# Optimization experiments

Measured on AMD Instinct MI355X. Metric: run time of the kernel, lower is better.

## Reference

```python
import jax, jax.numpy as jnp
import numpy as np

H = 1024          # hidden_size
NH = 16           # num_attention_heads
HD = H // NH      # attention_head_size
EPS = 1e-12       # layer_norm_eps
NEG = jnp.finfo(jnp.float32).min


def setup_inputs() -> dict:
    key = jax.random.key(0)
    ks = jax.random.split(key, 12)
    B, S = 4, 2048
    sc = 1.0 / np.sqrt(H)
    return {
        "hidden_states": jax.random.normal(ks[0], (B, S, H), jnp.float32),
        "attention_mask": jnp.ones((B, S), jnp.float32),
        "Wq": jax.random.normal(ks[1], (H, H), jnp.float32) * sc,
        "bq": jnp.zeros((H,), jnp.float32),
        "Wk": jax.random.normal(ks[2], (H, H), jnp.float32) * sc,
        "bk": jnp.zeros((H,), jnp.float32),
        "Wv": jax.random.normal(ks[3], (H, H), jnp.float32) * sc,
        "bv": jnp.zeros((H,), jnp.float32),
        "Wo": jax.random.normal(ks[4], (H, H), jnp.float32) * sc,
        "bo": jnp.zeros((H,), jnp.float32),
        "ln_g": jnp.ones((H,), jnp.float32),
        "ln_b": jnp.zeros((H,), jnp.float32),
    }


def _split_heads(x):
    # (B, S, H) -> (B, NH, S, HD)
    B, S, _ = x.shape
    return x.reshape(B, S, NH, HD).transpose(0, 2, 1, 3)


def reference(hidden_states, attention_mask, Wq, bq, Wk, bk, Wv, bv, Wo, bo, ln_g, ln_b):
    q = _split_heads(hidden_states @ Wq + bq)
    k = _split_heads(hidden_states @ Wk + bk)
    v = _split_heads(hidden_states @ Wv + bv)

    # (B, NH, S, S)
    scores = jnp.einsum('bhqd,bhkd->bhqk', q, k) / jnp.sqrt(jnp.float32(HD))
    mask_add = (1.0 - attention_mask)[:, None, None, :] * NEG
    scores = scores + mask_add
    probs = jax.nn.softmax(scores, axis=-1)  # dropout is identity (eval / p=0)

    ctx = jnp.einsum('bhqk,bhkd->bhqd', probs, v)
    B, _, S, _ = ctx.shape
    ctx = ctx.transpose(0, 2, 1, 3).reshape(B, S, H)

    out = ctx @ Wo + bo
    x = out + hidden_states
    mu = jnp.mean(x, axis=-1, keepdims=True)
    var = jnp.var(x, axis=-1, keepdims=True)
    return (x - mu) * jax.lax.rsqrt(var + EPS) * ln_g + ln_b
```

## Files before the change

kernel.cpp:

```cpp
#include <hip/hip_runtime.h>
#include <stdint.h>

#define H_ 1024
#define NH_ 16
#define HD_ 64
#define B_ 4
#define S_ 2048
#define M_ (B_*S_)

typedef unsigned short u16;
typedef __attribute__((ext_vector_type(4))) unsigned short u16x4;
typedef __attribute__((ext_vector_type(8))) short bf16x8;
typedef __attribute__((ext_vector_type(4))) float f32x4;
typedef __attribute__((ext_vector_type(16))) float f32x16;
typedef __attribute__((ext_vector_type(4))) unsigned int u32x4;
typedef __attribute__((ext_vector_type(4))) int i32x4;

#define AS1 __attribute__((address_space(1)))
#define AS3 __attribute__((address_space(3)))

__device__ __forceinline__ void gload16(const void* g, void* l) {
  __builtin_amdgcn_global_load_lds((const AS1 void*)g, (AS3 void*)l, 16, 0, 0);
}

__device__ __forceinline__ u16 f2bf(float f) {
  union { float f; uint32_t u; } v; v.f = f;
  uint32_t u = v.u + 0x7FFFu + ((v.u >> 16) & 1u);
  return (u16)(u >> 16);
}

static __device__ __forceinline__ f32x4 mfma16(bf16x8 a, bf16x8 b, f32x4 c) {
  return __builtin_amdgcn_mfma_f32_16x16x32_bf16(a, b, c, 0, 0, 0);
}
static __device__ __forceinline__ f32x16 mfma32(bf16x8 a, bf16x8 b, f32x16 c) {
  return __builtin_amdgcn_mfma_f32_32x32x16_bf16(a, b, c, 0, 0, 0);
}

__device__ __forceinline__ int cvtpk(float lo, float hi) {
  int r;
  asm("v_cvt_pk_bf16_f32 %0, %1, %2" : "=v"(r) : "v"(lo), "v"(hi));
  return r;
}
__device__ __forceinline__ void plswap(int& a, int& b) {
  asm volatile("v_permlane32_swap_b32 %0, %1" : "+v"(a), "+v"(b));
}
#if __has_builtin(__builtin_amdgcn_exp2f)
#define EXP2F __builtin_amdgcn_exp2f
#else
#define EXP2F exp2f
#endif

__device__ __forceinline__ int xcd_swz(int bid, int nwg) {
  return (bid & 7) * (nwg >> 3) + (bid >> 3);
}


__global__ __launch_bounds__(256) void prep_kernel(const float* __restrict__ in, u16* __restrict__ out,
                                                   const float* __restrict__ mask, float* __restrict__ madd_g,
                                                   uint32_t* __restrict__ nzbits,
                                                   const float* __restrict__ Wq, const float* __restrict__ Wk,
                                                   const float* __restrict__ Wv, const float* __restrict__ Wo,
                                                   u16* __restrict__ wt) {
  __shared__ float tile[64][65];
  const int bid = blockIdx.x, t = threadIdx.x;
  if (bid < 4096) {
    int i = bid * 256 + t;
    const f32x4* p = (const f32x4*)in;
    f32x4 a = p[2*i], b = p[2*i+1];
    u32x4 o;
    o.x = (uint32_t)f2bf(a.x) | ((uint32_t)f2bf(a.y) << 16);
    o.y = (uint32_t)f2bf(a.z) | ((uint32_t)f2bf(a.w) << 16);
    o.z = (uint32_t)f2bf(b.x) | ((uint32_t)f2bf(b.y) << 16);
    o.w = (uint32_t)f2bf(b.z) | ((uint32_t)f2bf(b.w) << 16);
    ((u32x4*)out)[i] = o;
  } else if (bid < 4100) {
    const int mb = bid - 4096;
    int i = mb * 256 + t;
    f32x4 a = ((const f32x4*)mask)[2*i], b4 = ((const f32x4*)mask)[2*i+1];
    f32x4 ma, mb4;
    ma.x = (1.0f - a.x) * -3.0e38f;  ma.y = (1.0f - a.y) * -3.0e38f;
    ma.z = (1.0f - a.z) * -3.0e38f;  ma.w = (1.0f - a.w) * -3.0e38f;
    mb4.x = (1.0f - b4.x) * -3.0e38f; mb4.y = (1.0f - b4.y) * -3.0e38f;
    mb4.z = (1.0f - b4.z) * -3.0e38f; mb4.w = (1.0f - b4.w) * -3.0e38f;
    ((f32x4*)madd_g)[2*i] = ma;  ((f32x4*)madd_g)[2*i+1] = mb4;
    if (mb == 0) {
      if (t < B_) nzbits[t] = 0u;
      __syncthreads();
      if (t < B_*32) {
        int b = t >> 5, kt = t & 31;
        const float* mrow = mask + (size_t)b * S_ + kt*64;
        uint32_t nz = 0;
        for (int c = 0; c < 64; ++c) nz |= (mrow[c] != 1.0f) ? 1u : 0u;
        if (nz) atomicOr(&nzbits[b], 1u << kt);
      }
    }
  } else {
    const int w = bid - 4100;
    const int p = w >> 8, ti = w & 255, tr = ti >> 4, tc = ti & 15;
    const float* W = (p == 0) ? Wq : (p == 1) ? Wk : (p == 2) ? Wv : Wo;
#pragma unroll
    for (int it = 0; it < 16; ++it) {
      int idx = it * 256 + t, r = idx >> 6, c = idx & 63;
      tile[r][c] = W[(size_t)(tr*64 + r) * H_ + tc*64 + c];
    }
    __syncthreads();
    u16* outp = wt + (size_t)p * H_ * H_;
#pragma unroll
    for (int it = 0; it < 16; ++it) {
      int idx = it * 256 + t, r = idx >> 6, c = idx & 63;
      outp[(size_t)(tc*64 + r) * H_ + tr*64 + c] = f2bf(tile[c][r]);
    }
  }
}


__device__ __forceinline__ void gemm_tile(const u16* __restrict__ A, const u16* __restrict__ Bt,
                                          int m0, int n0, u16* As, u16* Bs, f32x4 acc[4][4]) {
  const int tid = threadIdx.x;
  const int lane = tid & 63, wave = tid >> 6;
  const int wr = wave >> 1, wc = wave & 1;
  const int l15 = lane & 15, l4 = lane >> 4;
  const int rdx = l15 & 7;
#define GSTAGE(bb, k0) do { \
    _Pragma("unroll") \
    for (int i = 0; i < 4; ++i) { \
      int c = i*256 + tid, row = c >> 3, ch = c & 7; \
      int so = (k0) + ((ch ^ (row & 7)) * 8);    \
      gload16(A + (size_t)(m0 + row) * H_ + so, As + (bb)*8192 + (size_t)c * 8); \
      gload16(Bt + (size_t)(n0 + row) * H_ + so, Bs + (bb)*8192 + (size_t)c * 8); \
    } \
  } while (0)
  GSTAGE(0, 0);
  for (int kt = 0; kt < 16; ++kt) {
    const int cur = kt & 1;
    const int nk = ((kt + 1) & 15) * 64;
    GSTAGE(cur ^ 1, nk);
    asm volatile("s_waitcnt vmcnt(8)\n\ts_barrier" ::: "memory");
    const u16* Ab = As + cur*8192;
    const u16* Bb = Bs + cur*8192;
#pragma unroll
    for (int ks = 0; ks < 2; ++ks) {
      bf16x8 afr[4], bfr[4];
#pragma unroll
      for (int m = 0; m < 4; ++m)
        afr[m] = *(const bf16x8*)&Ab[(wr*64 + m*16 + l15)*64 + (((ks*4 + l4) ^ rdx) * 8)];
#pragma unroll
      for (int n = 0; n < 4; ++n)
        bfr[n] = *(const bf16x8*)&Bb[(wc*64 + n*16 + l15)*64 + (((ks*4 + l4) ^ rdx) * 8)];
#pragma unroll
      for (int m = 0; m < 4; ++m)
#pragma unroll
        for (int n = 0; n < 4; ++n)
          acc[m][n] = mfma16(afr[m], bfr[n], acc[m][n]);
    }
    asm volatile("s_barrier" ::: "memory");
  }
  asm volatile("s_waitcnt vmcnt(0)" ::: "memory");
#undef GSTAGE
}

__global__ __launch_bounds__(256) void gemm_qkv_kernel(const u16* __restrict__ hs16, const u16* __restrict__ wt,
                                                       const float* __restrict__ bq, const float* __restrict__ bk,
                                                       const float* __restrict__ bv, u16* __restrict__ qkv16) {
  __shared__ __align__(16) u16 As[2*128*64], Bs[2*128*64];
  f32x4 acc[4][4] = {};
  const int lg = xcd_swz(blockIdx.x, 1536);
  const int m0 = (lg / 24) * 128, n0 = (lg % 24) * 128;
  gemm_tile(hs16, wt, m0, n0, As, Bs, acc);
  const int tid = threadIdx.x, lane = tid & 63, wave = tid >> 6;
  const int wr = wave >> 1, wc = wave & 1, l15 = lane & 15, l4 = lane >> 4;
  const int p = n0 >> 10;
  const float* bias = (p == 0) ? bq : (p == 1) ? bk : bv;
  const float qsc = (p == 0) ? 0.18033688f : 1.0f;
  u16* base = qkv16 + (size_t)p * ((size_t)B_*NH_*S_*HD_);
  if (p == 2) {
    const int b = m0 >> 11;
#pragma unroll
    for (int n = 0; n < 4; ++n) {
      int ncol = (n0 & 1023) + wc*64 + n*16 + l15;
      int h = ncol >> 6, d = ncol & 63;
      float bsv = bias[ncol];
#pragma unroll
      for (int m = 0; m < 4; ++m) {
        int s0 = (m0 & 2047) + wr*64 + m*16 + l4*4;
        u16x4 pk;
#pragma unroll
        for (int r = 0; r < 4; ++r) pk[r] = f2bf(acc[m][n][r] + bsv);
        *(u16x4*)(base + (((size_t)b*NH_ + h)*HD_ + d)*S_ + s0) = pk;
      }
    }
  } else {
#pragma unroll
    for (int n = 0; n < 4; ++n) {
      int ncol = (n0 & 1023) + wc*64 + n*16 + l15;
      int h = ncol >> 6, d = ncol & 63;
      float bsv = bias[ncol];
#pragma unroll
      for (int m = 0; m < 4; ++m) {
#pragma unroll
        for (int r = 0; r < 4; ++r) {
          int row = m0 + wr*64 + m*16 + l4*4 + r;
          int b = row >> 11, s = row & 2047;
          base[(((size_t)b*NH_ + h)*S_ + s)*HD_ + d] = f2bf((acc[m][n][r] + bsv) * qsc);
        }
      }
    }
  }
}

__global__ __launch_bounds__(256) void gemm_out_kernel(const u16* __restrict__ ctx16, const u16* __restrict__ wo,
                                                       const float* __restrict__ bo, const float* __restrict__ hs,
                                                       float* __restrict__ xout) {
  __shared__ __align__(16) u16 As[2*128*64], Bs[2*128*64];
  f32x4 acc[4][4] = {};
  const int lg = xcd_swz(blockIdx.x, 512);
  const int m0 = (lg / 8) * 128, n0 = (lg % 8) * 128;
  gemm_tile(ctx16, wo, m0, n0, As, Bs, acc);
  const int tid = threadIdx.x, lane = tid & 63, wave = tid >> 6;
  const int wr = wave >> 1, wc = wave & 1, l15 = lane & 15, l4 = lane >> 4;
#pragma unroll
  for (int n = 0; n < 4; ++n) {
    int col = n0 + wc*64 + n*16 + l15;
    float bsv = bo[col];
#pragma unroll
    for (int m = 0; m < 4; ++m) {
#pragma unroll
      for (int r = 0; r < 4; ++r) {
        int row = m0 + wr*64 + m*16 + l4*4 + r;
        size_t off = (size_t)row * H_ + col;
        xout[off] = acc[m][n][r] + bsv + hs[off];
      }
    }
  }
}


__global__ __launch_bounds__(256, 2) void attn_kernel(const u16* __restrict__ q_, const u16* __restrict__ k_,
                                                      const u16* __restrict__ vt_, const float* __restrict__ madd_g,
                                                      const uint32_t* __restrict__ nzbits,
                                                      u16* __restrict__ ctx16) {
  __shared__ __align__(16) u16 Ks[2][64*64], Vs[2][64*64];
  __shared__ __align__(16) float Sc[4][64];
  const int lgid = xcd_swz(blockIdx.x, 512);
  const int qb = lgid & 7, bh = lgid >> 3, h = bh & 15, b = bh >> 4;
  const int tid = threadIdx.x, lane = tid & 63, wave = tid >> 6;
  const int l31 = lane & 31, hi = lane >> 5;
  const size_t headoff = ((size_t)b * NH_ + h) * ((size_t)S_ * HD_);
  const u16* Q  = q_ + headoff;
  const u16* K  = k_ + headoff;
  const u16* Vt = vt_ + headoff;
  const uint32_t nzb = nzbits[b];
  const int qbase = qb*256 + wave*64;
  bf16x8 qfA[4], qfB[4];
#pragma unroll
  for (int st = 0; st < 4; ++st) {
    qfA[st] = *(const bf16x8*)(Q + (size_t)(qbase + l31) * HD_ + st*16 + hi*8);
    qfB[st] = *(const bf16x8*)(Q + (size_t)(qbase + 32 + l31) * HD_ + st*16 + hi*8);
  }
  f32x16 O00 = {}, O01 = {}, O10 = {}, O11 = {};
  float lA = 0.f, lB = 0.f;
  const int srow = tid >> 3, sch = tid & 7;
  const int gch = sch ^ (srow & 7);
  const int swzA = l31 & 7;

#define STAGE(bb, kt) do { \
    const u16* Kt_ = K + (size_t)(kt) * 64 * HD_; \
    _Pragma("unroll") \
    for (int c = 0; c < 2; ++c) { \
      int row = c*32 + srow; \
      gload16(Kt_ + (size_t)row * HD_ + gch*8, &Ks[bb][c*2048 + (size_t)tid*8]); \
      gload16(Vt + (size_t)row * S_ + (kt)*64 + gch*8, &Vs[bb][c*2048 + (size_t)tid*8]); \
    } \
  } while (0)

  STAGE(0, 0);
  __syncthreads();

  for (int kt = 0; kt < 32; ++kt) {
    const int cur = kt & 1;
    const int nxt = (kt + 1) & 31;
    STAGE(cur ^ 1, nxt);
    asm volatile("s_waitcnt vmcnt(4)\n\ts_barrier" ::: "memory");
    f32x16 sA0 = {}, sA1 = {}, sB0 = {}, sB1 = {};
    __builtin_amdgcn_s_setprio(1);
#pragma unroll
    for (int st = 0; st < 4; ++st) {
      const int kch = ((2*st + hi) ^ swzA) * 8;
      bf16x8 kf0 = *(const bf16x8*)&Ks[cur][l31*64 + kch];
      bf16x8 kf1 = *(const bf16x8*)&Ks[cur][(32 + l31)*64 + kch];
      sA0 = mfma32(kf0, qfA[st], sA0);
      sA1 = mfma32(kf1, qfA[st], sA1);
      sB0 = mfma32(kf0, qfB[st], sB0);
      sB1 = mfma32(kf1, qfB[st], sB1);
    }
    __builtin_amdgcn_s_setprio(0);
    if ((nzb >> kt) & 1u) {
#pragma unroll
      for (int t = 0; t < 2; ++t) {
        f32x16& sa = t ? sA1 : sA0;
        f32x16& sb2 = t ? sB1 : sB0;
#pragma unroll
        for (int bq = 0; bq < 4; ++bq) {
          f32x4 md = *(const f32x4*)(madd_g + (size_t)b * S_ + kt*64 + t*32 + bq*8 + hi*4);
#pragma unroll
          for (int a = 0; a < 4; ++a) { sa[bq*4 + a] += md[a]; sb2[bq*4 + a] += md[a]; }
        }
      }
    }
#pragma unroll
    for (int r = 0; r < 16; ++r) sA0[r] = EXP2F(sA0[r]);
#pragma unroll
    for (int r = 0; r < 16; ++r) sA1[r] = EXP2F(sA1[r]);
#pragma unroll
    for (int r = 0; r < 16; ++r) sB0[r] = EXP2F(sB0[r]);
#pragma unroll
    for (int r = 0; r < 16; ++r) sB1[r] = EXP2F(sB1[r]);
    {
      float v[16];
#pragma unroll
      for (int r = 0; r < 16; ++r) v[r] = sA0[r] + sA1[r];
#pragma unroll
      for (int r = 0; r < 8; ++r) v[r] += v[r+8];
#pragma unroll
      for (int r = 0; r < 4; ++r) v[r] += v[r+4];
      float rs_ = (v[0] + v[1]) + (v[2] + v[3]);
      int a0 = __float_as_int(rs_), b0 = a0; plswap(a0, b0);
      lA += __int_as_float(a0) + __int_as_float(b0);
#pragma unroll
      for (int r = 0; r < 16; ++r) v[r] = sB0[r] + sB1[r];
#pragma unroll
      for (int r = 0; r < 8; ++r) v[r] += v[r+8];
#pragma unroll
      for (int r = 0; r < 4; ++r) v[r] += v[r+4];
      rs_ = (v[0] + v[1]) + (v[2] + v[3]);
      int a1 = __float_as_int(rs_), b1 = a1; plswap(a1, b1);
      lB += __int_as_float(a1) + __int_as_float(b1);
    }
    __builtin_amdgcn_s_setprio(1);
#pragma unroll
    for (int ks = 0; ks < 4; ++ks) {
      const f32x16& sa = (ks < 2) ? sA0 : sA1;
      const f32x16& sb2 = (ks < 2) ? sB0 : sB1;
      const int p = ks & 1;
      int pa0 = cvtpk(sa[8*p+0], sa[8*p+1]);
      int pa1 = cvtpk(sa[8*p+2], sa[8*p+3]);
      int pa2 = cvtpk(sa[8*p+4], sa[8*p+5]);
      int pa3 = cvtpk(sa[8*p+6], sa[8*p+7]);
      plswap(pa0, pa2); plswap(pa1, pa3);
      union { i32x4 i; bf16x8 hv; } ua; ua.i = (i32x4){pa0, pa1, pa2, pa3};
      int pb0 = cvtpk(sb2[8*p+0], sb2[8*p+1]);
      int pb1 = cvtpk(sb2[8*p+2], sb2[8*p+3]);
      int pb2 = cvtpk(sb2[8*p+4], sb2[8*p+5]);
      int pb3 = cvtpk(sb2[8*p+6], sb2[8*p+7]);
      plswap(pb0, pb2); plswap(pb1, pb3);
      union { i32x4 i; bf16x8 hv; } ub; ub.i = (i32x4){pb0, pb1, pb2, pb3};
      const int vch = ((2*ks + hi) ^ swzA) * 8;
      bf16x8 vb0 = *(const bf16x8*)&Vs[cur][l31*64 + vch];
      bf16x8 vb1 = *(const bf16x8*)&Vs[cur][(32 + l31)*64 + vch];
      O00 = mfma32(ua.hv, vb0, O00);
      O01 = mfma32(ua.hv, vb1, O01);
      O10 = mfma32(ub.hv, vb0, O10);
      O11 = mfma32(ub.hv, vb1, O11);
    }
    __builtin_amdgcn_s_setprio(0);
    asm volatile("s_barrier" ::: "memory");
  }
  asm volatile("s_waitcnt vmcnt(0)" ::: "memory");
  Sc[wave][l31]      = 1.0f / lA;
  Sc[wave][32 + l31] = 1.0f / lB;
#pragma unroll
  for (int bq = 0; bq < 4; ++bq) {
    f32x4 i0 = *(const f32x4*)&Sc[wave][bq*8 + hi*4];
    f32x4 i1 = *(const f32x4*)&Sc[wave][32 + bq*8 + hi*4];
#pragma unroll
    for (int a = 0; a < 4; ++a) {
      int ql = 8*bq + 4*hi + a, r = bq*4 + a;
      int sA_ = qbase + ql;
      size_t ob0 = ((size_t)(b * S_ + sA_) * NH_ + h) * HD_;
      ctx16[ob0 + l31]      = f2bf(O00[r] * i0[a]);
      ctx16[ob0 + 32 + l31] = f2bf(O01[r] * i0[a]);
      int sB_ = qbase + 32 + ql;
      size_t ob1 = ((size_t)(b * S_ + sB_) * NH_ + h) * HD_;
      ctx16[ob1 + l31]      = f2bf(O10[r] * i1[a]);
      ctx16[ob1 + 32 + l31] = f2bf(O11[r] * i1[a]);
    }
  }
#undef STAGE
}


__global__ __launch_bounds__(256) void ln_kernel(float* __restrict__ x, const float* __restrict__ g,
                                                 const float* __restrict__ bb) {
  const int row = blockIdx.x, t = threadIdx.x;
  float* xr = x + (size_t)row * H_;
  f32x4 v = ((const f32x4*)xr)[t];
  float s = v.x + v.y + v.z + v.w;
  float s2 = v.x*v.x + v.y*v.y + v.z*v.z + v.w*v.w;
#pragma unroll
  for (int o = 1; o < 64; o <<= 1) { s += __shfl_xor(s, o, 64); s2 += __shfl_xor(s2, o, 64); }
  __shared__ float red[8];
  const int wave = t >> 6, lane = t & 63;
  if (lane == 0) { red[wave] = s; red[4 + wave] = s2; }
  __syncthreads();
  s = red[0] + red[1] + red[2] + red[3];
  s2 = red[4] + red[5] + red[6] + red[7];
  const float mu = s * (1.0f / H_);
  const float var = s2 * (1.0f / H_) - mu * mu;
  const float rs = rsqrtf(var + 1e-12f);
  f32x4 gg = ((const f32x4*)g)[t], bb4 = ((const f32x4*)bb)[t];
  f32x4 o;
  o.x = (v.x - mu) * rs * gg.x + bb4.x;
  o.y = (v.y - mu) * rs * gg.y + bb4.y;
  o.z = (v.z - mu) * rs * gg.z + bb4.z;
  o.w = (v.w - mu) * rs * gg.w + bb4.w;
  ((f32x4*)xr)[t] = o;
}


extern "C" void kernel_launch(void* const* d_in, const int* in_sizes, int n_in,
                              void* d_out, int out_size, void* d_ws, size_t ws_size,
                              hipStream_t stream) {
  (void)in_sizes; (void)n_in; (void)out_size; (void)ws_size;
  const float* hs   = (const float*)d_in[0];
  const float* mask = (const float*)d_in[1];
  const float* Wq = (const float*)d_in[2];
  const float* bq = (const float*)d_in[3];
  const float* Wk = (const float*)d_in[4];
  const float* bk = (const float*)d_in[5];
  const float* Wv = (const float*)d_in[6];
  const float* bv = (const float*)d_in[7];
  const float* Wo = (const float*)d_in[8];
  const float* bo = (const float*)d_in[9];
  const float* lg = (const float*)d_in[10];
  const float* lb = (const float*)d_in[11];
  float* out = (float*)d_out;

  uint8_t* w = (uint8_t*)d_ws;
  u16* hs16  = (u16*)w;
  u16* wt16  = (u16*)(w + ((size_t)16 << 20));
  u16* qkv16 = (u16*)(w + ((size_t)24 << 20));
  u16* ctx16 = (u16*)(w + ((size_t)72 << 20));
  float* madd_g = (float*)(w + ((size_t)88 << 20));
  uint32_t* nzbits = (uint32_t*)(w + ((size_t)88 << 20) + 32768);

  const size_t psz = (size_t)B_*NH_*S_*HD_;
  prep_kernel<<<dim3(5124), dim3(256), 0, stream>>>(hs, hs16, mask, madd_g, nzbits,
                                                    Wq, Wk, Wv, Wo, wt16);
  gemm_qkv_kernel<<<dim3(1536), dim3(256), 0, stream>>>(hs16, wt16, bq, bk, bv, qkv16);
  attn_kernel<<<dim3(512), dim3(256), 0, stream>>>(qkv16, qkv16 + psz, qkv16 + 2*psz, madd_g, nzbits, ctx16);
  gemm_out_kernel<<<dim3(512), dim3(256), 0, stream>>>(ctx16, wt16 + (size_t)3*H_*H_, bo, hs, out);
  ln_kernel<<<dim3(M_), dim3(256), 0, stream>>>(out, lg, lb);
}
```

Baseline: 237.5 us.

## Restructure GEMM staging into four 32-wide K stages without swizzle

The shared GEMM tile routine now stages K in 32-element slices across four LDS buffers instead of two 64-element buffers. Each loop iteration prefetches two slices and computes on two. The XOR swizzle is dropped in favour of a plain row-major 32-wide layout with per-thread precomputed global pointers, which cuts address arithmetic. In exchange, LDS reads at a 64-byte row stride may hit more bank conflicts, and the vmcnt(8) wait now spans two stages' worth of loads.

```diff
diff --git a/kernel.cpp b/kernel.cpp
--- a/kernel.cpp
+++ b/kernel.cpp
@@ -120,49 +120,54 @@
   const int lane = tid & 63, wave = tid >> 6;
   const int wr = wave >> 1, wc = wave & 1;
   const int l15 = lane & 15, l4 = lane >> 4;
-  const int rdx = l15 & 7;
-#define GSTAGE(bb, k0) do { \
+  const int r0 = tid >> 2, c0 = (tid & 3) * 8;
+  const u16* Ap0 = A + (size_t)(m0 + r0) * H_ + c0;
+  const u16* Ap1 = A + (size_t)(m0 + 64 + r0) * H_ + c0;
+  const u16* Bp0 = Bt + (size_t)(n0 + r0) * H_ + c0;
+  const u16* Bp1 = Bt + (size_t)(n0 + 64 + r0) * H_ + c0;
+#define GSTAGE(ss, k0) do { \
+    gload16(Ap0 + (k0), As + (ss)*4096 + (size_t)tid * 8); \
+    gload16(Ap1 + (k0), As + (ss)*4096 + 2048 + (size_t)tid * 8); \
+    gload16(Bp0 + (k0), Bs + (ss)*4096 + (size_t)tid * 8); \
+    gload16(Bp1 + (k0), Bs + (ss)*4096 + 2048 + (size_t)tid * 8); \
+  } while (0)
+#define COMPUTE(ss) do { \
+    const u16* Ab = As + (ss)*4096; \
+    const u16* Bb = Bs + (ss)*4096; \
+    bf16x8 afr[4], bfr[4]; \
     _Pragma("unroll") \
-    for (int i = 0; i < 4; ++i) { \
-      int c = i*256 + tid, row = c >> 3, ch = c & 7; \
-      int so = (k0) + ((ch ^ (row & 7)) * 8);    \
-      gload16(A + (size_t)(m0 + row) * H_ + so, As + (bb)*8192 + (size_t)c * 8); \
-      gload16(Bt + (size_t)(n0 + row) * H_ + so, Bs + (bb)*8192 + (size_t)c * 8); \
-    } \
+    for (int m = 0; m < 4; ++m) afr[m] = *(const bf16x8*)&Ab[(wr*64 + m*16 + l15) * 32 + l4*8]; \
+    _Pragma("unroll") \
+    for (int n = 0; n < 4; ++n) bfr[n] = *(const bf16x8*)&Bb[(wc*64 + n*16 + l15) * 32 + l4*8]; \
+    _Pragma("unroll") \
+    for (int m = 0; m < 4; ++m) \
+      _Pragma("unroll") \
+      for (int n = 0; n < 4; ++n) \
+        acc[m][n] = mfma16(afr[m], bfr[n], acc[m][n]); \
   } while (0)
   GSTAGE(0, 0);
-  for (int kt = 0; kt < 16; ++kt) {
-    const int cur = kt & 1;
-    const int nk = ((kt + 1) & 15) * 64;
-    GSTAGE(cur ^ 1, nk);
+  GSTAGE(1, 32);
+  for (int it = 0; it < 16; ++it) {
+    const int s0 = (it*2) & 3, s1 = (it*2+1) & 3;
+    const int sa = (it*2+2) & 3, sb = (it*2+3) & 3;
+    const int ka = ((it*2+2) & 31) * 32;
+    const int kb = ((it*2+3) & 31) * 32;
+    GSTAGE(sa, ka);
+    GSTAGE(sb, kb);
     asm volatile("s_waitcnt vmcnt(8)\n\ts_barrier" ::: "memory");
-    const u16* Ab = As + cur*8192;
-    const u16* Bb = Bs + cur*8192;
-#pragma unroll
-    for (int ks = 0; ks < 2; ++ks) {
-      bf16x8 afr[4], bfr[4];
-#pragma unroll
-      for (int m = 0; m < 4; ++m)
-        afr[m] = *(const bf16x8*)&Ab[(wr*64 + m*16 + l15)*64 + (((ks*4 + l4) ^ rdx) * 8)];
-#pragma unroll
-      for (int n = 0; n < 4; ++n)
-        bfr[n] = *(const bf16x8*)&Bb[(wc*64 + n*16 + l15)*64 + (((ks*4 + l4) ^ rdx) * 8)];
-#pragma unroll
-      for (int m = 0; m < 4; ++m)
-#pragma unroll
-        for (int n = 0; n < 4; ++n)
-          acc[m][n] = mfma16(afr[m], bfr[n], acc[m][n]);
-    }
+    COMPUTE(s0);
+    COMPUTE(s1);
     asm volatile("s_barrier" ::: "memory");
   }
   asm volatile("s_waitcnt vmcnt(0)" ::: "memory");
 #undef GSTAGE
+#undef COMPUTE
 }
 
 __global__ __launch_bounds__(256) void gemm_qkv_kernel(const u16* __restrict__ hs16, const u16* __restrict__ wt,
                                                        const float* __restrict__ bq, const float* __restrict__ bk,
                                                        const float* __restrict__ bv, u16* __restrict__ qkv16) {
-  __shared__ __align__(16) u16 As[2*128*64], Bs[2*128*64];
+  __shared__ __align__(16) u16 As[4*128*32], Bs[4*128*32];
   f32x4 acc[4][4] = {};
   const int lg = xcd_swz(blockIdx.x, 1536);
   const int m0 = (lg / 24) * 128, n0 = (lg % 24) * 128;
@@ -211,7 +216,7 @@
 __global__ __launch_bounds__(256) void gemm_out_kernel(const u16* __restrict__ ctx16, const u16* __restrict__ wo,
                                                        const float* __restrict__ bo, const float* __restrict__ hs,
                                                        float* __restrict__ xout) {
-  __shared__ __align__(16) u16 As[2*128*64], Bs[2*128*64];
+  __shared__ __align__(16) u16 As[4*128*32], Bs[4*128*32];
   f32x4 acc[4][4] = {};
   const int lg = xcd_swz(blockIdx.x, 512);
   const int m0 = (lg / 8) * 128, n0 = (lg % 8) * 128;
```

New measurement: 251.7 us. 1.06x slower.
